# Performance work log

Measured on AMD Instinct MI355X. Metric: run time of the kernel, lower is better.

Reference implementation:

```python
import jax, jax.numpy as jnp
import numpy as np

B, S, DIN, DOUT, E, K = 4, 2048, 1024, 1024, 16, 2


def setup_inputs() -> dict:
    key = jax.random.key(0)
    ks = jax.random.split(key, 6)
    sc = 1.0 / np.sqrt(DIN)
    return {
        "x": jax.random.normal(ks[0], (B, S, DIN), jnp.float32),
        "gate_w": jax.random.uniform(ks[1], (DIN, E), jnp.float32, -sc, sc),
        "gate_b": jax.random.uniform(ks[2], (E,), jnp.float32, -sc, sc),
        "expert_w": jax.random.uniform(ks[3], (E, DIN, DOUT), jnp.float32, -sc, sc),
        "expert_b": jax.random.uniform(ks[4], (E, DOUT), jnp.float32, -sc, sc),
        "expert_biases": jnp.zeros((E,), jnp.float32),
    }


def reference(x, gate_w, gate_b, expert_w, expert_b, expert_biases):
    # gating
    gate_output = x @ gate_w + gate_b                 # [B,S,E]
    gate_probs = jax.nn.sigmoid(gate_output)          # [B,S,E]
    gate_logits = gate_output + expert_biases         # bias-corrected routing logits
    _, top_k_idx = jax.lax.top_k(gate_logits, K)      # [B,S,K] int32
    top_k_probs = jnp.take_along_axis(gate_probs, top_k_idx, axis=-1)  # [B,S,K]
    top_k_probs = top_k_probs / top_k_probs.sum(-1, keepdims=True)

    # dense all-expert compute, as in the original torch.stack
    expert_outputs = jnp.einsum('bsd,edf->ebsf', x, expert_w) + expert_b[:, None, None, :]  # [E,B,S,DOUT]

    # Faithful replication of the torch gather (which, due to the permute,
    # reads channel j (0..K-1) of the selected expert and broadcasts it over DOUT):
    # out[d,b,s,j] = expert_outputs[topk[b,s,j], b, s, j]
    b_ix = jnp.arange(B)[:, None, None]
    s_ix = jnp.arange(S)[None, :, None]
    j_ix = jnp.arange(K)[None, None, :]
    gathered = expert_outputs[top_k_idx, b_ix, s_ix, j_ix]  # [B,S,K]

    final_scalar = (gathered * top_k_probs).sum(-1)          # [B,S]
    final_output = jnp.broadcast_to(final_scalar[..., None], (B, S, DOUT))
    return final_output, gate_probs, top_k_idx
```

## Files before the change

### kernel.cpp

```cpp
#include <hip/hip_runtime.h>
#include <math.h>

#define DIN_  1024
#define DOUT_ 1024
#define NE    16
#define KK    2
#define NTOK  8192
#define RS4   257


__global__ __launch_bounds__(256) void compact_w_kernel(
    const float* __restrict__ ew,
    float* __restrict__ wc)
{
    int i = blockIdx.x * 256 + threadIdx.x;
    if (i >= NE * DIN_) return;
    int d = i & (DIN_ - 1);
    int e = i >> 10;
    const float2 v = *(const float2*)(ew + (size_t)e * DIN_ * DOUT_ + (size_t)d * DOUT_);
    wc[(size_t)e * KK * DIN_ + d]        = v.x;
    wc[(size_t)e * KK * DIN_ + DIN_ + d] = v.y;
}

__global__ __launch_bounds__(256) void fused_kernel(
    const float* __restrict__ x,
    const float* __restrict__ gate_w,
    const float* __restrict__ gate_b,
    const float* __restrict__ ebias,
    const float* __restrict__ wc,
    const float* __restrict__ expert_b,
    float* __restrict__ out_final,
    float* __restrict__ out_probs,
    float* __restrict__ out_idx,
    int write_aux)
{
    __shared__ float4 xs[16 * RS4];
    __shared__ float red2[4][16][17];
    __shared__ float lgt[16][17];
    __shared__ float4 recs[16];

    const int tid  = threadIdx.x;
    const int wave = tid >> 6;
    const int lane = tid & 63;
    const int blk  = blockIdx.x;

    const float4* xg = (const float4*)(x + (size_t)blk * 16 * DIN_);
#pragma unroll
    for (int k = 0; k < 16; k++) {
        int g = k * 256 + tid;
        xs[(g >> 8) * RS4 + (g & 255)] = xg[g];
    }
    __syncthreads();

    const int seg = tid >> 4;
    const int tok = tid & 15;
    const float4* xrow = xs + tok * RS4 + seg * 16;
    const float4* gw4  = (const float4*)gate_w;

    float acc[NE];
#pragma unroll
    for (int e = 0; e < NE; e++) acc[e] = 0.f;

    for (int i = 0; i < 16; i++) {
        float4 xv = xrow[i];
        int d0 = seg * 64 + i * 4;
#pragma unroll
        for (int j = 0; j < 4; j++) {
            int d = d0 + j;
            float xs_ = (j == 0) ? xv.x : (j == 1) ? xv.y : (j == 2) ? xv.z : xv.w;
            float4 g0 = gw4[d * 4 + 0];
            float4 g1 = gw4[d * 4 + 1];
            float4 g2 = gw4[d * 4 + 2];
            float4 g3 = gw4[d * 4 + 3];
            acc[0]  += xs_ * g0.x; acc[1]  += xs_ * g0.y; acc[2]  += xs_ * g0.z; acc[3]  += xs_ * g0.w;
            acc[4]  += xs_ * g1.x; acc[5]  += xs_ * g1.y; acc[6]  += xs_ * g1.z; acc[7]  += xs_ * g1.w;
            acc[8]  += xs_ * g2.x; acc[9]  += xs_ * g2.y; acc[10] += xs_ * g2.z; acc[11] += xs_ * g2.w;
            acc[12] += xs_ * g3.x; acc[13] += xs_ * g3.y; acc[14] += xs_ * g3.z; acc[15] += xs_ * g3.w;
        }
    }

#pragma unroll
    for (int e = 0; e < NE; e++) {
        acc[e] += __shfl_xor(acc[e], 16);
        acc[e] += __shfl_xor(acc[e], 32);
    }
    {
        const int q = seg & 3;
#pragma unroll
        for (int j = 0; j < 4; j++) {
            int e = q * 4 + j;
            red2[wave][tok][e] = acc[e];
        }
    }
    __syncthreads();

    {
        const int rtok = tid >> 4;
        const int e    = tid & 15;
        float s = red2[0][rtok][e] + red2[1][rtok][e]
                + red2[2][rtok][e] + red2[3][rtok][e] + gate_b[e];
        if (write_aux)
            out_probs[(size_t)(blk * 16 + rtok) * NE + e] = 1.f / (1.f + expf(-s));
        lgt[rtok][e] = s;
    }
    __syncthreads();

    if (tid < 16) {
        const int ftok = tid;
        const int gtoken = blk * 16 + ftok;
        float go[NE], logit[NE];
#pragma unroll
        for (int e = 0; e < NE; e++) {
            go[e] = lgt[ftok][e];
            logit[e] = go[e] + ebias[e];
        }
        int i0 = 0;
        for (int e = 1; e < NE; e++) if (logit[e] > logit[i0]) i0 = e;
        int i1 = -1;
        for (int e = 0; e < NE; e++) {
            if (e == i0) continue;
            if (i1 < 0 || logit[e] > logit[i1]) i1 = e;
        }
        float p0 = 1.f / (1.f + expf(-go[i0]));
        float p1 = 1.f / (1.f + expf(-go[i1]));
        float inv = 1.f / (p0 + p1);
        if (write_aux) {
            out_idx[(size_t)gtoken * KK + 0] = (float)i0;
            out_idx[(size_t)gtoken * KK + 1] = (float)i1;
        }
        recs[ftok] = make_float4((float)i0, (float)i1, p0 * inv, p1 * inv);
    }
    __syncthreads();

#pragma unroll
    for (int it = 0; it < 4; it++) {
        const int lt = wave * 4 + it;
        float4 rec = recs[lt];
        int e0 = (int)rec.x;
        int e1 = (int)rec.y;
        const float4* xr = xs + lt * RS4;
        const float4* w0 = (const float4*)(wc + ((size_t)e0 * KK + 0) * DIN_);
        const float4* w1 = (const float4*)(wc + ((size_t)e1 * KK + 1) * DIN_);
        float g0 = 0.f, g1 = 0.f;
#pragma unroll
        for (int i = 0; i < 4; i++) {
            float4 xv = xr[i * 64 + lane];
            float4 a  = w0[i * 64 + lane];
            float4 b  = w1[i * 64 + lane];
            g0 += xv.x * a.x + xv.y * a.y + xv.z * a.z + xv.w * a.w;
            g1 += xv.x * b.x + xv.y * b.y + xv.z * b.z + xv.w * b.w;
        }
#pragma unroll
        for (int m = 32; m >= 1; m >>= 1) {
            g0 += __shfl_xor(g0, m);
            g1 += __shfl_xor(g1, m);
        }
        float f = rec.z * (g0 + expert_b[(size_t)e0 * DOUT_ + 0])
                + rec.w * (g1 + expert_b[(size_t)e1 * DOUT_ + 1]);
        float4 fv = make_float4(f, f, f, f);
        float4* o4 = (float4*)(out_final + (size_t)(blk * 16 + lt) * DOUT_);
#pragma unroll
        for (int i = 0; i < 4; i++) o4[i * 64 + lane] = fv;
    }
}

extern "C" void kernel_launch(void* const* d_in, const int* in_sizes, int n_in,
                              void* d_out, int out_size, void* d_ws, size_t ws_size,
                              hipStream_t stream) {
    const float* x        = (const float*)d_in[0];
    const float* gate_w   = (const float*)d_in[1];
    const float* gate_b   = (const float*)d_in[2];
    const float* expert_w = (const float*)d_in[3];
    const float* expert_b = (const float*)d_in[4];
    const float* ebias    = (const float*)d_in[5];
    float* out = (float*)d_out;

    float* wc = (float*)d_ws;

    float* out_final = out;
    float* out_probs = out + (size_t)NTOK * DOUT_;
    float* out_idx   = out_probs + (size_t)NTOK * NE;
    int write_aux = (out_size >= NTOK * DOUT_ + NTOK * NE + NTOK * KK) ? 1 : 0;

    compact_w_kernel<<<(NE * DIN_ + 255) / 256, 256, 0, stream>>>(expert_w, wc);
    fused_kernel<<<NTOK / 16, 256, 0, stream>>>(
        x, gate_w, gate_b, ebias, wc, expert_b,
        out_final, out_probs, out_idx, write_aux);
}
```

Baseline: 148.9 us.

## Halve tokens per block and use nontemporal loads/stores for streaming data

Reduces tokens per block from 16 to 8, doubling the grid to 1024 blocks and halving LDS use per block so more blocks can be resident. The gate-matmul thread mapping and reduction are reworked to match, with an extra shuffle step. Streaming reads of x and expert weights and the broadcast output writes become nontemporal to avoid polluting the cache. The trade-off is that gate_w and the compacted weights are re-read by twice as many blocks.

New measurement: 146.7 us. About the same (-1.5%).

```diff
diff --git a/kernel.cpp b/kernel.cpp
--- a/kernel.cpp
+++ b/kernel.cpp
@@ -6,7 +6,11 @@
 #define NE    16
 #define KK    2
 #define NTOK  8192
+#define TPB   8
 #define RS4   257
+
+typedef float nf2 __attribute__((ext_vector_type(2)));
+typedef float nf4 __attribute__((ext_vector_type(4)));
 
 
 __global__ __launch_bounds__(256) void compact_w_kernel(
@@ -17,7 +21,8 @@
     if (i >= NE * DIN_) return;
     int d = i & (DIN_ - 1);
     int e = i >> 10;
-    const float2 v = *(const float2*)(ew + (size_t)e * DIN_ * DOUT_ + (size_t)d * DOUT_);
+    const nf2 v = __builtin_nontemporal_load(
+        (const nf2*)(ew + (size_t)e * DIN_ * DOUT_ + (size_t)d * DOUT_));
     wc[(size_t)e * KK * DIN_ + d]        = v.x;
     wc[(size_t)e * KK * DIN_ + DIN_ + d] = v.y;
 }
@@ -34,36 +39,38 @@
     float* __restrict__ out_idx,
     int write_aux)
 {
-    __shared__ float4 xs[16 * RS4];
-    __shared__ float red2[4][16][17];
-    __shared__ float lgt[16][17];
-    __shared__ float4 recs[16];
+    __shared__ float4 xs[TPB * RS4];
+    __shared__ float red2[4][TPB][17];
+    __shared__ float lgt[TPB][17];
+    __shared__ float4 recs[TPB];
 
     const int tid  = threadIdx.x;
     const int wave = tid >> 6;
     const int lane = tid & 63;
     const int blk  = blockIdx.x;
 
-    const float4* xg = (const float4*)(x + (size_t)blk * 16 * DIN_);
+    const nf4* xg = (const nf4*)(x + (size_t)blk * TPB * DIN_);
 #pragma unroll
-    for (int k = 0; k < 16; k++) {
+    for (int k = 0; k < 8; k++) {
         int g = k * 256 + tid;
-        xs[(g >> 8) * RS4 + (g & 255)] = xg[g];
+        nf4 v = __builtin_nontemporal_load(&xg[g]);
+        xs[(g >> 8) * RS4 + (g & 255)] = make_float4(v.x, v.y, v.z, v.w);
     }
     __syncthreads();
 
-    const int seg = tid >> 4;
-    const int tok = tid & 15;
-    const float4* xrow = xs + tok * RS4 + seg * 16;
+    const int seg = tid >> 3;
+    const int tok = tid & 7;
+    const float4* xrow = xs + tok * RS4 + seg * 8;
     const float4* gw4  = (const float4*)gate_w;
 
     float acc[NE];
 #pragma unroll
     for (int e = 0; e < NE; e++) acc[e] = 0.f;
 
-    for (int i = 0; i < 16; i++) {
+#pragma unroll
+    for (int i = 0; i < 8; i++) {
         float4 xv = xrow[i];
-        int d0 = seg * 64 + i * 4;
+        int d0 = seg * 32 + i * 4;
 #pragma unroll
         for (int j = 0; j < 4; j++) {
             int d = d0 + j;
@@ -81,33 +88,31 @@
 
 #pragma unroll
     for (int e = 0; e < NE; e++) {
+        acc[e] += __shfl_xor(acc[e], 8);
         acc[e] += __shfl_xor(acc[e], 16);
         acc[e] += __shfl_xor(acc[e], 32);
     }
     {
-        const int q = seg & 3;
-#pragma unroll
-        for (int j = 0; j < 4; j++) {
-            int e = q * 4 + j;
-            red2[wave][tok][e] = acc[e];
-        }
+        const int q = seg & 7;
+        red2[wave][tok][q * 2 + 0] = acc[q * 2 + 0];
+        red2[wave][tok][q * 2 + 1] = acc[q * 2 + 1];
     }
     __syncthreads();
 
-    {
+    if (tid < TPB * NE) {
         const int rtok = tid >> 4;
         const int e    = tid & 15;
         float s = red2[0][rtok][e] + red2[1][rtok][e]
                 + red2[2][rtok][e] + red2[3][rtok][e] + gate_b[e];
         if (write_aux)
-            out_probs[(size_t)(blk * 16 + rtok) * NE + e] = 1.f / (1.f + expf(-s));
+            out_probs[(size_t)(blk * TPB + rtok) * NE + e] = 1.f / (1.f + expf(-s));
         lgt[rtok][e] = s;
     }
     __syncthreads();
 
-    if (tid < 16) {
+    if (tid < TPB) {
         const int ftok = tid;
-        const int gtoken = blk * 16 + ftok;
+        const int gtoken = blk * TPB + ftok;
         float go[NE], logit[NE];
 #pragma unroll
         for (int e = 0; e < NE; e++) {
@@ -133,8 +138,8 @@
     __syncthreads();
 
 #pragma unroll
-    for (int it = 0; it < 4; it++) {
-        const int lt = wave * 4 + it;
+    for (int it = 0; it < 2; it++) {
+        const int lt = wave * 2 + it;
         float4 rec = recs[lt];
         int e0 = (int)rec.x;
         int e1 = (int)rec.y;
@@ -157,10 +162,11 @@
         }
         float f = rec.z * (g0 + expert_b[(size_t)e0 * DOUT_ + 0])
                 + rec.w * (g1 + expert_b[(size_t)e1 * DOUT_ + 1]);
-        float4 fv = make_float4(f, f, f, f);
-        float4* o4 = (float4*)(out_final + (size_t)(blk * 16 + lt) * DOUT_);
+        nf4 fv = {f, f, f, f};
+        nf4* o4 = (nf4*)(out_final + (size_t)(blk * TPB + lt) * DOUT_);
 #pragma unroll
-        for (int i = 0; i < 4; i++) o4[i * 64 + lane] = fv;
+        for (int i = 0; i < 4; i++)
+            __builtin_nontemporal_store(fv, &o4[i * 64 + lane]);
     }
 }
 
@@ -183,7 +189,7 @@
     int write_aux = (out_size >= NTOK * DOUT_ + NTOK * NE + NTOK * KK) ? 1 : 0;
 
     compact_w_kernel<<<(NE * DIN_ + 255) / 256, 256, 0, stream>>>(expert_w, wc);
-    fused_kernel<<<NTOK / 16, 256, 0, stream>>>(
+    fused_kernel<<<NTOK / TPB, 256, 0, stream>>>(
         x, gate_w, gate_b, ebias, wc, expert_b,
         out_final, out_probs, out_idx, write_aux);
 }
```
